# Kernel tuning notes

Measured on AMD Instinct MI355X. Metric: run time of the kernel, lower is better.

The kernel has to match this reference:

```python
import jax, jax.numpy as jnp
import numpy as np

TOP_K = 2


def setup_inputs() -> dict:
    key = jax.random.key(0)
    k0, k1, k2, k3, k4, k5 = jax.random.split(key, 6)
    N, D_IN, D_OUT, H, G = 8192, 1024, 1024, 4096, 3
    E = 2 ** G
    x = jax.random.normal(k0, (N, D_IN), jnp.float32)
    # gate: Linear(in_dim, gate_dim, bias=False) followed by act (ReLU)
    Wg = jax.random.normal(k1, (D_IN, G), jnp.float32) * (1.0 / np.sqrt(D_IN))
    # experts: per-expert 2-layer MLP: Linear(in,hid) + ReLU + Linear(hid,out)
    W1 = jax.random.normal(k2, (E, D_IN, H), jnp.float32) * (1.0 / np.sqrt(D_IN))
    b1 = jax.random.normal(k3, (E, H), jnp.float32) * 0.01
    W2 = jax.random.normal(k4, (E, H, D_OUT), jnp.float32) * (1.0 / np.sqrt(H))
    b2 = jax.random.normal(k5, (E, D_OUT), jnp.float32) * 0.01
    return {"x": x, "Wg": Wg, "W1": W1, "b1": b1, "W2": W2, "b2": b2}


def _hypercube_mask(E, G, dtype):
    # binary(arange(2^G), G) * 2 - 1 : corners of the hypercube in {-1,+1}^G
    codes = jnp.arange(E)
    bits = (codes[:, None] >> jnp.arange(G)[None, :]) & 1  # [E, G]
    return (bits * 2 - 1).astype(dtype)


def reference(x, Wg, W1, b1, W2, b2):
    G = Wg.shape[1]
    E = W1.shape[0]
    N = x.shape[0]
    mask = _hypercube_mask(E, G, x.dtype)                 # [E, G]
    logits = jax.nn.relu(x @ Wg)                          # [N, G]
    scores = logits @ mask.T                              # [N, E] = sum_d logits*mask
    probs = jax.nn.softmax(scores, axis=1)                # softmax over experts
    topv, topi = jax.lax.top_k(probs, TOP_K)              # [N, k]
    topv = topv / topv.sum(axis=-1, keepdims=True)        # renormalize selected probs
    # dense combine weights: zero for non-selected experts (same math as gather/scatter dispatch)
    combine = jnp.zeros((N, E), x.dtype).at[jnp.arange(N)[:, None], topi].set(topv)
    out = jnp.zeros((N, W2.shape[2]), x.dtype)
    for e in range(E):  # small fixed expert count
        h = jax.nn.relu(x @ W1[e] + b1[e])                # [N, H]
        out = out + combine[:, e:e + 1] * (h @ W2[e] + b2[e])
    return out
```

## Files before the change

kernel.cpp:

```cpp
#include <hip/hip_runtime.h>

#define NTOK 8192
#define DIN  1024
#define DOUT 1024
#define HDIM 4096
#define NEXP 8
#define NPAIR (NTOK * 2)

typedef __attribute__((ext_vector_type(8))) short bf16x8;
typedef __attribute__((ext_vector_type(4))) float f32x4;

__device__ __forceinline__ unsigned short f2bf(float f) {
  union { float f; unsigned u; } v; v.f = f;
  unsigned u = v.u;
  unsigned r = (u + 0x7fffu + ((u >> 16) & 1u)) >> 16;
  return (unsigned short)r;
}

__device__ __forceinline__ void gload16(const void* g, void* l) {
  __builtin_amdgcn_global_load_lds(
      (const __attribute__((address_space(1))) unsigned int*)g,
      (__attribute__((address_space(3))) unsigned int*)l, 16, 0, 0);
}

__global__ void gate_kernel(const float* __restrict__ x, const float* __restrict__ Wg,
                            int* __restrict__ cnt, int* __restrict__ ptok,
                            float* __restrict__ pw) {
  const int lane = threadIdx.x & 63;
  const int t = blockIdx.x * 4 + (threadIdx.x >> 6);
  const float* xr = x + (size_t)t * DIN + lane * 16;
  const float* wr = Wg + (size_t)lane * 16 * 3;
  double d0 = 0, d1 = 0, d2 = 0;
#pragma unroll
  for (int j = 0; j < 16; j++) {
    double xv = xr[j];
    d0 += xv * wr[j * 3 + 0];
    d1 += xv * wr[j * 3 + 1];
    d2 += xv * wr[j * 3 + 2];
  }
#pragma unroll
  for (int o = 32; o > 0; o >>= 1) {
    d0 += __shfl_down(d0, o);
    d1 += __shfl_down(d1, o);
    d2 += __shfl_down(d2, o);
  }
  if (lane == 0) {
    double l0 = d0 > 0 ? d0 : 0, l1 = d1 > 0 ? d1 : 0, l2 = d2 > 0 ? d2 : 0;
    double s[NEXP];
#pragma unroll
    for (int e = 0; e < NEXP; e++)
      s[e] = ((e & 1) ? l0 : -l0) + ((e & 2) ? l1 : -l1) + ((e & 4) ? l2 : -l2);
    int e0 = 0;
    for (int e = 1; e < NEXP; e++) if (s[e] > s[e0]) e0 = e;
    int e1 = -1;
    for (int e = 0; e < NEXP; e++) { if (e == e0) continue; if (e1 < 0 || s[e] > s[e1]) e1 = e; }
    double w0 = 1.0 / (1.0 + exp(s[e1] - s[e0]));
    double w1 = 1.0 - w0;
    int p0 = atomicAdd(cnt + e0, 1);
    ptok[e0 * NTOK + p0] = t; pw[e0 * NTOK + p0] = (float)w0;
    int p1 = atomicAdd(cnt + e1, 1);
    ptok[e1 * NTOK + p1] = t; pw[e1 * NTOK + p1] = (float)w1;
  }
}

__global__ void scan_kernel(const int* __restrict__ cnt, int* __restrict__ off) {
  if (threadIdx.x == 0) {
    int a = 0;
    for (int e = 0; e < NEXP; e++) { off[e] = a; a += cnt[e]; }
  }
}

__global__ void cvt_bf16_kernel(const float* __restrict__ src,
                                unsigned short* __restrict__ dst, int n) {
  int i = (blockIdx.x * 256 + threadIdx.x) * 8;
  if (i >= n) return;
  float4 a = *(const float4*)(src + i);
  float4 b = *(const float4*)(src + i + 4);
  __align__(16) unsigned short t[8] = {f2bf(a.x), f2bf(a.y), f2bf(a.z), f2bf(a.w),
                                       f2bf(b.x), f2bf(b.y), f2bf(b.z), f2bf(b.w)};
  *(uint4*)(dst + i) = *(const uint4*)t;
}

__global__ void transpose_cvt(const float* __restrict__ src,
                              unsigned short* __restrict__ dst, int K, int N) {
  __shared__ float tile[64][65];
  const size_t base = (size_t)blockIdx.z * K * N;
  const float* s = src + base;
  unsigned short* d = dst + base;
  int n0 = blockIdx.x * 64, k0 = blockIdx.y * 64;
  for (int idx = threadIdx.x; idx < 64 * 16; idx += 256) {
    int r = idx >> 4, c4 = (idx & 15) * 4;
    float4 v = *(const float4*)(s + (size_t)(k0 + r) * N + n0 + c4);
    tile[r][c4 + 0] = v.x; tile[r][c4 + 1] = v.y;
    tile[r][c4 + 2] = v.z; tile[r][c4 + 3] = v.w;
  }
  __syncthreads();
  for (int idx = threadIdx.x; idx < 64 * 8; idx += 256) {
    int nl = idx >> 3, c8 = (idx & 7) * 8;
    __align__(16) unsigned short tmp[8];
#pragma unroll
    for (int j = 0; j < 8; j++) tmp[j] = f2bf(tile[c8 + j][nl]);
    *(uint4*)(d + (size_t)(n0 + nl) * K + k0 + c8) = *(const uint4*)tmp;
  }
}

__global__ __launch_bounds__(1024, 2) void gemm1_kernel(
    const unsigned short* __restrict__ xbf,
    const unsigned short* __restrict__ w1t,
    const float* __restrict__ b1,
    const int* __restrict__ cnt, const int* __restrict__ off,
    const int* __restrict__ ptok,
    unsigned short* __restrict__ h)
{
  const int bid = blockIdx.x;
  const int e = bid & 7;
  const int ce = cnt[e];
  const int idx = bid >> 3;
  const int mt = idx >> 4;
  const int nt = idx & 15;
  const int m0 = mt * 256;
  if (m0 >= ce) return;
  const int n0 = nt * 256;
  const int oe = off[e];
  __shared__ __align__(16) unsigned short lA[2][256 * 32];
  __shared__ __align__(16) unsigned short lB[2][256 * 32];
  const int tid = threadIdx.x;
  const int lane = tid & 63;
  const int wv = tid >> 6;
  const int wr = wv >> 2, wc = wv & 3;

  const int ra = tid >> 2;
  const int ka = (tid & 3) * 8;
  const int ta = ptok[e * NTOK + min(m0 + ra, ce - 1)];
  const unsigned short* ga = xbf + (size_t)ta * DIN + ka;
  const unsigned short* wb = w1t + (size_t)e * HDIM * DIN;
  const unsigned short* gb = wb + (size_t)(n0 + ra) * DIN + ka;

  f32x4 acc[4][4] = {};
  const int fr = lane & 15;
  const int fk = (lane >> 4) * 8;

#define STAGE1(buf, kk)                          \
  do {                                           \
    gload16(ga + (kk), &lA[buf][tid * 8]);       \
    gload16(gb + (kk), &lB[buf][tid * 8]);       \
  } while (0)

#define COMPUTE1(buf)                                                        \
  do {                                                                       \
    bf16x8 a[4], b[4];                                                       \
    _Pragma("unroll") for (int i = 0; i < 4; i++)                            \
      a[i] = *(const bf16x8*)(&lA[buf][(wr * 64 + i * 16 + fr) * 32 + fk]);  \
    _Pragma("unroll") for (int i = 0; i < 4; i++)                            \
      b[i] = *(const bf16x8*)(&lB[buf][(wc * 64 + i * 16 + fr) * 32 + fk]);  \
    _Pragma("unroll") for (int mi = 0; mi < 4; mi++)                         \
      _Pragma("unroll") for (int ni = 0; ni < 4; ni++)                       \
        acc[mi][ni] = __builtin_amdgcn_mfma_f32_16x16x32_bf16(               \
            a[mi], b[ni], acc[mi][ni], 0, 0, 0);                             \
  } while (0)

  STAGE1(0, 0);
  asm volatile("s_waitcnt vmcnt(0)" ::: "memory");
  __syncthreads();
  int cur = 0;
  for (int k0 = 32; k0 < DIN; k0 += 32) {
    STAGE1(cur ^ 1, k0);
    COMPUTE1(cur);
    asm volatile("s_waitcnt vmcnt(0)" ::: "memory");
    __syncthreads();
    cur ^= 1;
  }
  COMPUTE1(cur);

  const int cr = (lane >> 4) * 4;
  const int cc = lane & 15;
#pragma unroll
  for (int mi = 0; mi < 4; mi++) {
    int rbase = wr * 64 + mi * 16 + cr;
#pragma unroll
    for (int r = 0; r < 4; r++) {
      int grow = m0 + rbase + r;
      if (grow >= ce) continue;
      size_t hoff = (size_t)(oe + grow) * HDIM;
#pragma unroll
      for (int ni = 0; ni < 4; ni++) {
        int col = n0 + wc * 64 + ni * 16 + cc;
        float v = acc[mi][ni][r] + b1[e * HDIM + col];
        h[hoff + col] = f2bf(v > 0.f ? v : 0.f);
      }
    }
  }
}

__global__ __launch_bounds__(1024, 2) void gemm2_kernel(
    const unsigned short* __restrict__ h,
    const unsigned short* __restrict__ w2t,
    const float* __restrict__ b2,
    const int* __restrict__ cnt, const int* __restrict__ off,
    const int* __restrict__ ptok, const float* __restrict__ pw,
    float* __restrict__ out)
{
  const int bid = blockIdx.x;
  const int e = bid & 7;
  const int ce = cnt[e];
  const int idx = bid >> 3;
  const int mt = idx >> 2;
  const int nt = idx & 3;
  const int m0 = mt * 256;
  if (m0 >= ce) return;
  const int n0 = nt * 256;
  const int oe = off[e];
  __shared__ __align__(16) unsigned short lA[2][256 * 32];
  __shared__ __align__(16) unsigned short lB[2][256 * 32];
  const int tid = threadIdx.x;
  const int lane = tid & 63;
  const int wv = tid >> 6;
  const int wr = wv >> 2, wc = wv & 3;

  const int ra = tid >> 2;
  const int ka = (tid & 3) * 8;
  const int rc = min(m0 + ra, ce - 1);
  const unsigned short* ga = h + (size_t)(oe + rc) * HDIM + ka;
  const unsigned short* wbp = w2t + (size_t)e * DOUT * HDIM;
  const unsigned short* gb = wbp + (size_t)(n0 + ra) * HDIM + ka;

  f32x4 acc[4][4] = {};
  const int fr = lane & 15;
  const int fk = (lane >> 4) * 8;

#define STAGE2(buf, kk)                          \
  do {                                           \
    gload16(ga + (kk), &lA[buf][tid * 8]);       \
    gload16(gb + (kk), &lB[buf][tid * 8]);       \
  } while (0)

#define COMPUTE2(buf)                                                        \
  do {                                                                       \
    bf16x8 a[4], b[4];                                                       \
    _Pragma("unroll") for (int i = 0; i < 4; i++)                            \
      a[i] = *(const bf16x8*)(&lA[buf][(wr * 64 + i * 16 + fr) * 32 + fk]);  \
    _Pragma("unroll") for (int i = 0; i < 4; i++)                            \
      b[i] = *(const bf16x8*)(&lB[buf][(wc * 64 + i * 16 + fr) * 32 + fk]);  \
    _Pragma("unroll") for (int mi = 0; mi < 4; mi++)                         \
      _Pragma("unroll") for (int ni = 0; ni < 4; ni++)                       \
        acc[mi][ni] = __builtin_amdgcn_mfma_f32_16x16x32_bf16(               \
            a[mi], b[ni], acc[mi][ni], 0, 0, 0);                             \
  } while (0)

  STAGE2(0, 0);
  asm volatile("s_waitcnt vmcnt(0)" ::: "memory");
  __syncthreads();
  int cur = 0;
  for (int k0 = 32; k0 < HDIM; k0 += 32) {
    STAGE2(cur ^ 1, k0);
    COMPUTE2(cur);
    asm volatile("s_waitcnt vmcnt(0)" ::: "memory");
    __syncthreads();
    cur ^= 1;
  }
  COMPUTE2(cur);

  const int cr = (lane >> 4) * 4;
  const int cc = lane & 15;
#pragma unroll
  for (int mi = 0; mi < 4; mi++) {
    int rbase = wr * 64 + mi * 16 + cr;
#pragma unroll
    for (int r = 0; r < 4; r++) {
      int grow = m0 + rbase + r;
      if (grow >= ce) continue;
      int pidx = e * NTOK + grow;
      int token = ptok[pidx];
      float w = pw[pidx];
#pragma unroll
      for (int ni = 0; ni < 4; ni++) {
        int col = n0 + wc * 64 + ni * 16 + cc;
        float v = (acc[mi][ni][r] + b2[e * DOUT + col]) * w;
        atomicAdd(out + (size_t)token * DOUT + col, v);
      }
    }
  }
}

extern "C" void kernel_launch(void* const* d_in, const int* in_sizes, int n_in,
                              void* d_out, int out_size, void* d_ws, size_t ws_size,
                              hipStream_t stream) {
  const float* x  = (const float*)d_in[0];
  const float* Wg = (const float*)d_in[1];
  const float* W1 = (const float*)d_in[2];
  const float* b1 = (const float*)d_in[3];
  const float* W2 = (const float*)d_in[4];
  const float* b2 = (const float*)d_in[5];
  float* out = (float*)d_out;

  char* ws = (char*)d_ws;
  size_t o = 0;
  auto nxt = [&](size_t b) { char* p = ws + o; o = (o + b + 255) & ~(size_t)255; return p; };
  int* cnt = (int*)nxt(64);
  int* off = (int*)nxt(64);
  int* ptok = (int*)nxt((size_t)NEXP * NTOK * 4);
  float* pw = (float*)nxt((size_t)NEXP * NTOK * 4);
  unsigned short* xbf = (unsigned short*)nxt((size_t)NTOK * DIN * 2);
  unsigned short* w1t = (unsigned short*)nxt((size_t)NEXP * HDIM * DIN * 2);
  unsigned short* w2t = (unsigned short*)nxt((size_t)NEXP * DOUT * HDIM * 2);
  unsigned short* hbuf = (unsigned short*)nxt((size_t)NPAIR * HDIM * 2);

  hipMemsetAsync(cnt, 0, 64, stream);
  hipMemsetAsync(out, 0, (size_t)NTOK * DOUT * 4, stream);

  gate_kernel<<<NTOK / 4, 256, 0, stream>>>(x, Wg, cnt, ptok, pw);
  scan_kernel<<<1, 64, 0, stream>>>(cnt, off);
  cvt_bf16_kernel<<<(NTOK * DIN / 8) / 256, 256, 0, stream>>>(x, xbf, NTOK * DIN);
  transpose_cvt<<<dim3(HDIM / 64, DIN / 64, NEXP), 256, 0, stream>>>(W1, w1t, DIN, HDIM);
  transpose_cvt<<<dim3(DOUT / 64, HDIM / 64, NEXP), 256, 0, stream>>>(W2, w2t, HDIM, DOUT);

  gemm1_kernel<<<8 * (NTOK / 256) * (HDIM / 256), 1024, 0, stream>>>(
      xbf, w1t, b1, cnt, off, ptok, hbuf);
  gemm2_kernel<<<8 * (NTOK / 256) * (DOUT / 256), 1024, 0, stream>>>(
      hbuf, w2t, b2, cnt, off, ptok, pw, out);
}
```

Measured before the change: 984.3 us.

## Restructure expert GEMMs into 8-wave ping-pong pipeline with swizzled 64-wide K tiles

Both expert GEMM kernels move from 16 waves with a 32-wide K step to 8 waves, each holding a 128x64 accumulator tile. K tiles are now 64 wide and staged into 128KB of dynamic LDS with an XOR swizzle to avoid bank conflicts. The main loop is split into four phases that interleave global-to-LDS loads with MFMA quadrants, using barriers, sched_barrier and setprio so memory and compute overlap. The cost is more registers per wave, one block per CU, and many hand-placed barriers that make the schedule fragile.

```diff
diff --git a/kernel.cpp b/kernel.cpp
--- a/kernel.cpp
+++ b/kernel.cpp
@@ -104,7 +104,53 @@
   }
 }
 
-__global__ __launch_bounds__(1024, 2) void gemm1_kernel(
+
+#define RD_A(qm, bufb)                                                         \
+  _Pragma("unroll") for (int fi = 0; fi < 4; fi++)                             \
+    _Pragma("unroll") for (int ks = 0; ks < 2; ks++)                           \
+      areg[fi][ks] = *(const bf16x8*)(lds + (bufb) +                           \
+          (unsigned)((rowA_base + (qm) * 64 + fi * 16) * 128 +                 \
+                     ((ks * 64 + hi * 16) ^ cxor)));
+
+#define RD_B(qn, breg, bufb)                                                   \
+  _Pragma("unroll") for (int fj = 0; fj < 2; fj++)                             \
+    _Pragma("unroll") for (int ks = 0; ks < 2; ks++)                           \
+      breg[fj][ks] = *(const bf16x8*)(lds + (bufb) + 32768u +                  \
+          (unsigned)((rowB_base + (qn) * 32 + fj * 16) * 128 +                 \
+                     ((ks * 64 + hi * 16) ^ cxor)));
+
+#define MM_Q(qm, qn, breg)                                                     \
+  _Pragma("unroll") for (int fi = 0; fi < 4; fi++)                             \
+    _Pragma("unroll") for (int fj = 0; fj < 2; fj++)                           \
+      _Pragma("unroll") for (int ks = 0; ks < 2; ks++)                         \
+        acc[(qm) * 4 + fi][(qn) * 2 + fj] =                                    \
+            __builtin_amdgcn_mfma_f32_16x16x32_bf16(                           \
+                areg[fi][ks], breg[fj][ks], acc[(qm) * 4 + fi][(qn) * 2 + fj], \
+                0, 0, 0);
+
+#define STG(hh, bv, kel)                                                       \
+  do {                                                                         \
+    unsigned db = (unsigned)(bv) * 65536u +                                    \
+                  (((hh) < 2) ? (unsigned)(hh) * 16384u                        \
+                              : 32768u + (unsigned)((hh) - 2) * 16384u);       \
+    const unsigned short* s0 = ((hh) < 2) ? aptr[(hh) * 2] : bptr[((hh) - 2) * 2];         \
+    const unsigned short* s1 = ((hh) < 2) ? aptr[(hh) * 2 + 1] : bptr[((hh) - 2) * 2 + 1]; \
+    gload16(s0 + (kel), lds + db + (unsigned)tid * 16u);                       \
+    gload16(s1 + (kel), lds + db + 8192u + (unsigned)tid * 16u);               \
+  } while (0)
+
+#define PH_TOP(hh)                                                             \
+  if (more) STG(hh, bufn, kel);
+
+#define PH_MFMA(qm, qn, breg)                                                  \
+  __builtin_amdgcn_s_barrier();                                                \
+  __builtin_amdgcn_sched_barrier(0);                                           \
+  __builtin_amdgcn_s_setprio(1);                                               \
+  MM_Q(qm, qn, breg);                                                          \
+  __builtin_amdgcn_s_setprio(0);                                               \
+  __builtin_amdgcn_sched_barrier(0);
+
+__global__ __launch_bounds__(512, 1) void gemm1_kernel(
     const unsigned short* __restrict__ xbf,
     const unsigned short* __restrict__ w1t,
     const float* __restrict__ b1,
@@ -112,6 +158,7 @@
     const int* __restrict__ ptok,
     unsigned short* __restrict__ h)
 {
+  extern __shared__ char lds[];
   const int bid = blockIdx.x;
   const int e = bid & 7;
   const int ce = cnt[e];
@@ -122,77 +169,89 @@
   if (m0 >= ce) return;
   const int n0 = nt * 256;
   const int oe = off[e];
-  __shared__ __align__(16) unsigned short lA[2][256 * 32];
-  __shared__ __align__(16) unsigned short lB[2][256 * 32];
   const int tid = threadIdx.x;
   const int lane = tid & 63;
-  const int wv = tid >> 6;
-  const int wr = wv >> 2, wc = wv & 3;
-
-  const int ra = tid >> 2;
-  const int ka = (tid & 3) * 8;
-  const int ta = ptok[e * NTOK + min(m0 + ra, ce - 1)];
-  const unsigned short* ga = xbf + (size_t)ta * DIN + ka;
+  const int wid = tid >> 6;
+  const int wm = wid >> 2;
+  const int wn = wid & 3;
+
+  const int kofs = ((tid & 7) * 8) ^ (((tid >> 3) & 7) << 3);
+  const int rth = tid >> 3;
+  const unsigned short* aptr[4];
+  const unsigned short* bptr[4];
   const unsigned short* wb = w1t + (size_t)e * HDIM * DIN;
-  const unsigned short* gb = wb + (size_t)(n0 + ra) * DIN + ka;
-
-  f32x4 acc[4][4] = {};
+#pragma unroll
+  for (int i = 0; i < 4; i++) {
+    int r = rth + i * 64;
+    int ta = ptok[e * NTOK + min(m0 + r, ce - 1)];
+    aptr[i] = xbf + (size_t)ta * DIN + kofs;
+    bptr[i] = wb + (size_t)(n0 + r) * DIN + kofs;
+  }
+
   const int fr = lane & 15;
-  const int fk = (lane >> 4) * 8;
-
-#define STAGE1(buf, kk)                          \
-  do {                                           \
-    gload16(ga + (kk), &lA[buf][tid * 8]);       \
-    gload16(gb + (kk), &lB[buf][tid * 8]);       \
-  } while (0)
-
-#define COMPUTE1(buf)                                                        \
-  do {                                                                       \
-    bf16x8 a[4], b[4];                                                       \
-    _Pragma("unroll") for (int i = 0; i < 4; i++)                            \
-      a[i] = *(const bf16x8*)(&lA[buf][(wr * 64 + i * 16 + fr) * 32 + fk]);  \
-    _Pragma("unroll") for (int i = 0; i < 4; i++)                            \
-      b[i] = *(const bf16x8*)(&lB[buf][(wc * 64 + i * 16 + fr) * 32 + fk]);  \
-    _Pragma("unroll") for (int mi = 0; mi < 4; mi++)                         \
-      _Pragma("unroll") for (int ni = 0; ni < 4; ni++)                       \
-        acc[mi][ni] = __builtin_amdgcn_mfma_f32_16x16x32_bf16(               \
-            a[mi], b[ni], acc[mi][ni], 0, 0, 0);                             \
-  } while (0)
-
-  STAGE1(0, 0);
-  asm volatile("s_waitcnt vmcnt(0)" ::: "memory");
-  __syncthreads();
-  int cur = 0;
-  for (int k0 = 32; k0 < DIN; k0 += 32) {
-    STAGE1(cur ^ 1, k0);
-    COMPUTE1(cur);
-    asm volatile("s_waitcnt vmcnt(0)" ::: "memory");
-    __syncthreads();
-    cur ^= 1;
-  }
-  COMPUTE1(cur);
-
-  const int cr = (lane >> 4) * 4;
-  const int cc = lane & 15;
-#pragma unroll
-  for (int mi = 0; mi < 4; mi++) {
-    int rbase = wr * 64 + mi * 16 + cr;
+  const int hi = lane >> 4;
+  const int cxor = (fr & 7) << 4;
+  const int rowA_base = wm * 128 + fr;
+  const int rowB_base = wn * 64 + fr;
+
+  f32x4 acc[8][4] = {};
+  bf16x8 areg[4][2], b0reg[2][2], b1reg[2][2];
+
+  {
+    const bool more = true; const int bufn = 0; const int kel = 0;
+    PH_TOP(0); PH_TOP(1); PH_TOP(2); PH_TOP(3);
+  }
+
+  const int KT = DIN / 64;
+  for (int t = 0; t < KT; t++) {
+    const unsigned bb = (unsigned)(t & 1) * 65536u;
+    const int bufn = (t + 1) & 1;
+    const int kel = (t + 1) * 64;
+    const bool more = (t + 1 < KT);
+    PH_TOP(0);
+    if (more) asm volatile("s_waitcnt vmcnt(2)" ::: "memory");
+    else      asm volatile("s_waitcnt vmcnt(0)" ::: "memory");
+    __builtin_amdgcn_s_barrier();
+    __builtin_amdgcn_sched_barrier(0);
+    RD_A(0, bb); RD_B(0, b0reg, bb); RD_B(1, b1reg, bb);
+    __builtin_amdgcn_sched_barrier(0);
+    __builtin_amdgcn_s_setprio(1);
+    MM_Q(0, 0, b0reg);
+    __builtin_amdgcn_s_setprio(0);
+    __builtin_amdgcn_sched_barrier(0);
+    __builtin_amdgcn_s_barrier();
+    PH_TOP(1);
+    PH_MFMA(0, 1, b1reg);
+    RD_A(1, bb);
+    __builtin_amdgcn_sched_barrier(0);
+    __builtin_amdgcn_s_barrier();
+    PH_TOP(2);
+    PH_MFMA(1, 1, b1reg);
+    __builtin_amdgcn_s_barrier();
+    PH_TOP(3);
+    PH_MFMA(1, 0, b0reg);
+    __builtin_amdgcn_s_barrier();
+  }
+
+#pragma unroll
+  for (int am = 0; am < 8; am++) {
+    int rbase = wm * 128 + am * 16 + hi * 4;
 #pragma unroll
     for (int r = 0; r < 4; r++) {
       int grow = m0 + rbase + r;
       if (grow >= ce) continue;
       size_t hoff = (size_t)(oe + grow) * HDIM;
 #pragma unroll
-      for (int ni = 0; ni < 4; ni++) {
-        int col = n0 + wc * 64 + ni * 16 + cc;
-        float v = acc[mi][ni][r] + b1[e * HDIM + col];
+      for (int an = 0; an < 4; an++) {
+        int col = n0 + wn * 64 + an * 16 + fr;
+        float v = acc[am][an][r] + b1[e * HDIM + col];
         h[hoff + col] = f2bf(v > 0.f ? v : 0.f);
       }
     }
   }
 }
 
-__global__ __launch_bounds__(1024, 2) void gemm2_kernel(
+__global__ __launch_bounds__(512, 1) void gemm2_kernel(
     const unsigned short* __restrict__ h,
     const unsigned short* __restrict__ w2t,
     const float* __restrict__ b2,
@@ -200,6 +259,7 @@
     const int* __restrict__ ptok, const float* __restrict__ pw,
     float* __restrict__ out)
 {
+  extern __shared__ char lds[];
   const int bid = blockIdx.x;
   const int e = bid & 7;
   const int ce = cnt[e];
@@ -210,61 +270,73 @@
   if (m0 >= ce) return;
   const int n0 = nt * 256;
   const int oe = off[e];
-  __shared__ __align__(16) unsigned short lA[2][256 * 32];
-  __shared__ __align__(16) unsigned short lB[2][256 * 32];
   const int tid = threadIdx.x;
   const int lane = tid & 63;
-  const int wv = tid >> 6;
-  const int wr = wv >> 2, wc = wv & 3;
-
-  const int ra = tid >> 2;
-  const int ka = (tid & 3) * 8;
-  const int rc = min(m0 + ra, ce - 1);
-  const unsigned short* ga = h + (size_t)(oe + rc) * HDIM + ka;
-  const unsigned short* wbp = w2t + (size_t)e * DOUT * HDIM;
-  const unsigned short* gb = wbp + (size_t)(n0 + ra) * HDIM + ka;
-
-  f32x4 acc[4][4] = {};
+  const int wid = tid >> 6;
+  const int wm = wid >> 2;
+  const int wn = wid & 3;
+
+  const int kofs = ((tid & 7) * 8) ^ (((tid >> 3) & 7) << 3);
+  const int rth = tid >> 3;
+  const unsigned short* aptr[4];
+  const unsigned short* bptr[4];
+  const unsigned short* wb = w2t + (size_t)e * DOUT * HDIM;
+#pragma unroll
+  for (int i = 0; i < 4; i++) {
+    int r = rth + i * 64;
+    int rc = min(m0 + r, ce - 1);
+    aptr[i] = h + (size_t)(oe + rc) * HDIM + kofs;
+    bptr[i] = wb + (size_t)(n0 + r) * HDIM + kofs;
+  }
+
   const int fr = lane & 15;
-  const int fk = (lane >> 4) * 8;
-
-#define STAGE2(buf, kk)                          \
-  do {                                           \
-    gload16(ga + (kk), &lA[buf][tid * 8]);       \
-    gload16(gb + (kk), &lB[buf][tid * 8]);       \
-  } while (0)
-
-#define COMPUTE2(buf)                                                        \
-  do {                                                                       \
-    bf16x8 a[4], b[4];                                                       \
-    _Pragma("unroll") for (int i = 0; i < 4; i++)                            \
-      a[i] = *(const bf16x8*)(&lA[buf][(wr * 64 + i * 16 + fr) * 32 + fk]);  \
-    _Pragma("unroll") for (int i = 0; i < 4; i++)                            \
-      b[i] = *(const bf16x8*)(&lB[buf][(wc * 64 + i * 16 + fr) * 32 + fk]);  \
-    _Pragma("unroll") for (int mi = 0; mi < 4; mi++)                         \
-      _Pragma("unroll") for (int ni = 0; ni < 4; ni++)                       \
-        acc[mi][ni] = __builtin_amdgcn_mfma_f32_16x16x32_bf16(               \
-            a[mi], b[ni], acc[mi][ni], 0, 0, 0);                             \
-  } while (0)
-
-  STAGE2(0, 0);
-  asm volatile("s_waitcnt vmcnt(0)" ::: "memory");
-  __syncthreads();
-  int cur = 0;
-  for (int k0 = 32; k0 < HDIM; k0 += 32) {
-    STAGE2(cur ^ 1, k0);
-    COMPUTE2(cur);
-    asm volatile("s_waitcnt vmcnt(0)" ::: "memory");
-    __syncthreads();
-    cur ^= 1;
-  }
-  COMPUTE2(cur);
-
-  const int cr = (lane >> 4) * 4;
-  const int cc = lane & 15;
-#pragma unroll
-  for (int mi = 0; mi < 4; mi++) {
-    int rbase = wr * 64 + mi * 16 + cr;
+  const int hi = lane >> 4;
+  const int cxor = (fr & 7) << 4;
+  const int rowA_base = wm * 128 + fr;
+  const int rowB_base = wn * 64 + fr;
+
+  f32x4 acc[8][4] = {};
+  bf16x8 areg[4][2], b0reg[2][2], b1reg[2][2];
+
+  {
+    const bool more = true; const int bufn = 0; const int kel = 0;
+    PH_TOP(0); PH_TOP(1); PH_TOP(2); PH_TOP(3);
+  }
+
+  const int KT = HDIM / 64;
+  for (int t = 0; t < KT; t++) {
+    const unsigned bb = (unsigned)(t & 1) * 65536u;
+    const int bufn = (t + 1) & 1;
+    const int kel = (t + 1) * 64;
+    const bool more = (t + 1 < KT);
+    PH_TOP(0);
+    if (more) asm volatile("s_waitcnt vmcnt(2)" ::: "memory");
+    else      asm volatile("s_waitcnt vmcnt(0)" ::: "memory");
+    __builtin_amdgcn_s_barrier();
+    __builtin_amdgcn_sched_barrier(0);
+    RD_A(0, bb); RD_B(0, b0reg, bb); RD_B(1, b1reg, bb);
+    __builtin_amdgcn_sched_barrier(0);
+    __builtin_amdgcn_s_setprio(1);
+    MM_Q(0, 0, b0reg);
+    __builtin_amdgcn_s_setprio(0);
+    __builtin_amdgcn_sched_barrier(0);
+    __builtin_amdgcn_s_barrier();
+    PH_TOP(1);
+    PH_MFMA(0, 1, b1reg);
+    RD_A(1, bb);
+    __builtin_amdgcn_sched_barrier(0);
+    __builtin_amdgcn_s_barrier();
+    PH_TOP(2);
+    PH_MFMA(1, 1, b1reg);
+    __builtin_amdgcn_s_barrier();
+    PH_TOP(3);
+    PH_MFMA(1, 0, b0reg);
+    __builtin_amdgcn_s_barrier();
+  }
+
+#pragma unroll
+  for (int am = 0; am < 8; am++) {
+    int rbase = wm * 128 + am * 16 + hi * 4;
 #pragma unroll
     for (int r = 0; r < 4; r++) {
       int grow = m0 + rbase + r;
@@ -273,9 +345,9 @@
       int token = ptok[pidx];
       float w = pw[pidx];
 #pragma unroll
-      for (int ni = 0; ni < 4; ni++) {
-        int col = n0 + wc * 64 + ni * 16 + cc;
-        float v = (acc[mi][ni][r] + b2[e * DOUT + col]) * w;
+      for (int an = 0; an < 4; an++) {
+        int col = n0 + wn * 64 + an * 16 + fr;
+        float v = (acc[am][an][r] + b2[e * DOUT + col]) * w;
         atomicAdd(out + (size_t)token * DOUT + col, v);
       }
     }
@@ -305,6 +377,11 @@
   unsigned short* w2t = (unsigned short*)nxt((size_t)NEXP * DOUT * HDIM * 2);
   unsigned short* hbuf = (unsigned short*)nxt((size_t)NPAIR * HDIM * 2);
 
+  hipFuncSetAttribute((const void*)gemm1_kernel,
+                      hipFuncAttributeMaxDynamicSharedMemorySize, 131072);
+  hipFuncSetAttribute((const void*)gemm2_kernel,
+                      hipFuncAttributeMaxDynamicSharedMemorySize, 131072);
+
   hipMemsetAsync(cnt, 0, 64, stream);
   hipMemsetAsync(out, 0, (size_t)NTOK * DOUT * 4, stream);
 
@@ -314,8 +391,8 @@
   transpose_cvt<<<dim3(HDIM / 64, DIN / 64, NEXP), 256, 0, stream>>>(W1, w1t, DIN, HDIM);
   transpose_cvt<<<dim3(DOUT / 64, HDIM / 64, NEXP), 256, 0, stream>>>(W2, w2t, HDIM, DOUT);
 
-  gemm1_kernel<<<8 * (NTOK / 256) * (HDIM / 256), 1024, 0, stream>>>(
+  gemm1_kernel<<<8 * (NTOK / 256) * (HDIM / 256), 512, 131072, stream>>>(
       xbf, w1t, b1, cnt, off, ptok, hbuf);
-  gemm2_kernel<<<8 * (NTOK / 256) * (DOUT / 256), 1024, 0, stream>>>(
+  gemm2_kernel<<<8 * (NTOK / 256) * (DOUT / 256), 512, 131072, stream>>>(
       hbuf, w2t, b2, cnt, off, ptok, pw, out);
 }
```

New measurement: 901.3 us. 8.4% less time.
